# Performance work log

Measured on AMD Instinct MI355X. Metric: run time of the kernel, lower is better.

## Reference

```python
import jax, jax.numpy as jnp
import numpy as np


def setup_inputs() -> dict:
    key = jax.random.key(0)
    k1, k2, k3, k4 = jax.random.split(key, 4)
    B, T, D, U = 64, 2048, 256, 256
    X = jax.random.normal(k1, (B, T, D), dtype=jnp.float32)
    # scale weights ~ Glorot-ish so activations stay in range
    kernel = jax.random.normal(k2, (D, 3 * U), dtype=jnp.float32) / np.sqrt(D)
    recurrent_kernel = jax.random.normal(k3, (U, 3 * U), dtype=jnp.float32) / np.sqrt(U)
    bias = jax.random.normal(k4, (3 * U,), dtype=jnp.float32) * 0.01
    return {"X": X, "kernel": kernel, "recurrent_kernel": recurrent_kernel, "bias": bias}


def reference(X, kernel, recurrent_kernel, bias):
    # X: [B, T, D]; kernel: [D, 3U]; recurrent_kernel: [U, 3U]; bias: [3U]
    U = recurrent_kernel.shape[0]
    B = X.shape[0]
    Uz = recurrent_kernel[:, :U]
    Ur = recurrent_kernel[:, U:2 * U]
    Uh = recurrent_kernel[:, 2 * U:]
    # Precompute input projections for all timesteps in one GEMM (same math
    # as per-step matmul(x, W*) + B*).
    proj = X @ kernel + bias            # [B, T, 3U]
    proj = jnp.swapaxes(proj, 0, 1)     # [T, B, 3U] for scan over time
    xz = proj[:, :, :U]
    xr = proj[:, :, U:2 * U]
    xh = proj[:, :, 2 * U:]

    def step(a, xs):
        tz, tr, th = xs                  # each [B, U]
        z = jax.nn.sigmoid(a @ Uz + tz)
        r = jax.nn.sigmoid(a @ Ur + tr)
        h = jnp.tanh((r * a) @ Uh + th)
        a = z * a + (1.0 - z) * h
        return a, None

    a0 = jnp.zeros((B, U), dtype=X.dtype)
    a_final, _ = jax.lax.scan(step, a0, (xz, xr, xh))
    return a_final  # [B, U]
```

## Files before the change

### kernel.cpp

```cpp
#include <hip/hip_runtime.h>


typedef _Float16 half2_t __attribute__((ext_vector_type(2)));
typedef _Float16 half8_t __attribute__((ext_vector_type(8)));
typedef float    float4_t __attribute__((ext_vector_type(4)));

#define T_LEN 2048
#define B_SZ  64
#define D_IN  256
#define N3    768
#define U_SZ  256

#define H2(v, p) __builtin_shufflevector((v), (v), 2*(p), 2*(p)+1)

__device__ __forceinline__ float fdot2f(half2_t a, half2_t b, float c) {
#if __has_builtin(__builtin_amdgcn_fdot2)
    return __builtin_amdgcn_fdot2(a, b, c, false);
#else
    return c + (float)a[0]*(float)b[0] + (float)a[1]*(float)b[1];
#endif
}

__device__ __forceinline__ float fast_sigmoid(float s) {
    return __builtin_amdgcn_rcpf(1.0f + __builtin_amdgcn_exp2f(-1.44269504f * s));
}
__device__ __forceinline__ float fast_tanh(float s) {
    return 1.0f - 2.0f * __builtin_amdgcn_rcpf(1.0f + __builtin_amdgcn_exp2f(2.88539008f * s));
}

#define GA_LD 264
#define NT_N  16
#define MT_M  2048

__global__ __launch_bounds__(256) void proj_gemm(
    const float* __restrict__ X, const float* __restrict__ W,
    const float* __restrict__ bias, _Float16* __restrict__ proj)
{
    __shared__ __align__(16) _Float16 Ah[64 * GA_LD];
    __shared__ __align__(16) _Float16 Wh[48 * GA_LD];

    unsigned bid = blockIdx.x;
    unsigned idx = bid >> 3;
    unsigned mt  = (bid & 7) * (MT_M / 8) + (idx >> 4);
    unsigned nt  = idx & (NT_N - 1);
    int m0 = mt * 64, n0 = nt * 48;
    int tid = threadIdx.x;

    {
        int r = tid >> 6;
        int k = (tid & 63) * 4;
        #pragma unroll
        for (int i = 0; i < 16; ++i) {
            int row = i * 4 + r;
            float4_t v = *(const float4_t*)(X + (size_t)(m0 + row) * D_IN + k);
            _Float16* p = Ah + row * GA_LD + k;
            p[0] = (_Float16)v.x; p[1] = (_Float16)v.y;
            p[2] = (_Float16)v.z; p[3] = (_Float16)v.w;
        }
    }
    {
        int c  = tid & 63;
        int kk = tid >> 6;
        if (c < 48) {
            #pragma unroll 4
            for (int i = 0; i < 64; ++i) {
                int krow = i * 4 + kk;
                Wh[c * GA_LD + krow] = (_Float16)W[(size_t)krow * N3 + n0 + c];
            }
        }
    }
    __syncthreads();

    int r0 = (tid >> 4) << 2;
    int c  = tid & 15;
    float acc[4][3];
    #pragma unroll
    for (int rr = 0; rr < 4; ++rr)
        #pragma unroll
        for (int cc = 0; cc < 3; ++cc) acc[rr][cc] = 0.0f;

    for (int j = 0; j < 32; ++j) {
        half8_t av[4], wv[3];
        #pragma unroll
        for (int rr = 0; rr < 4; ++rr)
            av[rr] = *(const half8_t*)(Ah + (r0 + rr) * GA_LD + j * 8);
        #pragma unroll
        for (int cc = 0; cc < 3; ++cc)
            wv[cc] = *(const half8_t*)(Wh + (c + 16 * cc) * GA_LD + j * 8);
        #pragma unroll
        for (int rr = 0; rr < 4; ++rr)
            #pragma unroll
            for (int cc = 0; cc < 3; ++cc) {
                acc[rr][cc] = fdot2f(H2(av[rr],0), H2(wv[cc],0), acc[rr][cc]);
                acc[rr][cc] = fdot2f(H2(av[rr],1), H2(wv[cc],1), acc[rr][cc]);
                acc[rr][cc] = fdot2f(H2(av[rr],2), H2(wv[cc],2), acc[rr][cc]);
                acc[rr][cc] = fdot2f(H2(av[rr],3), H2(wv[cc],3), acc[rr][cc]);
            }
    }

    float bv[3];
    #pragma unroll
    for (int cc = 0; cc < 3; ++cc) bv[cc] = bias[n0 + c + 16 * cc];
    #pragma unroll
    for (int rr = 0; rr < 4; ++rr)
        #pragma unroll
        for (int cc = 0; cc < 3; ++cc)
            proj[(size_t)(m0 + r0 + rr) * N3 + (n0 + c + 16 * cc)] =
                (_Float16)(acc[rr][cc] + bv[cc]);
}

__global__ __launch_bounds__(768) void gru_scan(
    const float* __restrict__ RK, const _Float16* __restrict__ proj,
    float* __restrict__ out)
{
    __shared__ __align__(16) _Float16 aH[U_SZ];
    __shared__ __align__(16) _Float16 raH[U_SZ];
    __shared__ float zS[U_SZ];
    __shared__ float aF[U_SZ];

    const int b   = blockIdx.x;
    const int tid = threadIdx.x;
    const int g   = tid >> 8;
    const int u   = tid & 255;

    half2_t wcol[128];
    {
        const float* wp = RK + (size_t)(g << 8) + u;
        #pragma unroll
        for (int k2 = 0; k2 < 128; ++k2) {
            half2_t h;
            h[0] = (_Float16)wp[(size_t)(2 * k2)     * N3];
            h[1] = (_Float16)wp[(size_t)(2 * k2 + 1) * N3];
            wcol[k2] = h;
        }
    }

    if (tid < U_SZ) { aF[tid] = 0.0f; aH[tid] = (_Float16)0.0f; }

    const _Float16* px = proj + ((size_t)b * T_LEN) * N3 + (g << 8) + u;
    float xv = (float)px[0];
    __syncthreads();

    for (int t = 0; t < T_LEN; ++t) {
        const float x_cur = xv;
        if (t + 1 < T_LEN) xv = (float)px[(size_t)(t + 1) * N3];

        if (g < 2) {
            float acc = 0.0f;
            #pragma unroll
            for (int j = 0; j < 32; ++j) {
                half8_t av = *(const half8_t*)(aH + j * 8);
                acc = fdot2f(H2(av,0), wcol[4*j+0], acc);
                acc = fdot2f(H2(av,1), wcol[4*j+1], acc);
                acc = fdot2f(H2(av,2), wcol[4*j+2], acc);
                acc = fdot2f(H2(av,3), wcol[4*j+3], acc);
            }
            float sig = fast_sigmoid(acc + x_cur);
            if (g == 0) zS[u]  = sig;
            else        raH[u] = (_Float16)(sig * aF[u]);
        }
        __syncthreads();

        if (g == 2) {
            float acc = 0.0f;
            #pragma unroll
            for (int j = 0; j < 32; ++j) {
                half8_t rv = *(const half8_t*)(raH + j * 8);
                acc = fdot2f(H2(rv,0), wcol[4*j+0], acc);
                acc = fdot2f(H2(rv,1), wcol[4*j+1], acc);
                acc = fdot2f(H2(rv,2), wcol[4*j+2], acc);
                acc = fdot2f(H2(rv,3), wcol[4*j+3], acc);
            }
            float h  = fast_tanh(acc + x_cur);
            float z  = zS[u];
            float an = z * aF[u] + (1.0f - z) * h;
            aF[u] = an;
            aH[u] = (_Float16)an;
        }
        __syncthreads();
    }

    if (g == 0) out[(size_t)b * U_SZ + u] = aF[u];
}

extern "C" void kernel_launch(void* const* d_in, const int* in_sizes, int n_in,
                              void* d_out, int out_size, void* d_ws, size_t ws_size,
                              hipStream_t stream)
{
    const float* X    = (const float*)d_in[0];
    const float* W    = (const float*)d_in[1];
    const float* RK   = (const float*)d_in[2];
    const float* bias = (const float*)d_in[3];
    _Float16* proj = (_Float16*)d_ws;

    proj_gemm<<<MT_M * NT_N, 256, 0, stream>>>(X, W, bias, proj);
    gru_scan<<<B_SZ, 768, 0, stream>>>(RK, proj, (float*)d_out);
}
```

Before: 3.911 ms.

## Split candidate-gate matvec across all threads with K-halving and shuffle reduction

The GRU scan drops from 768 to 512 threads. In phase 2 every thread now computes half of the candidate-gate dot product (128 K-elements) and pairs combine their halves with a lane shuffle, so the third group no longer serializes the Uh matvec while two-thirds of threads idle. Accumulation also uses four independent partial sums to shorten fdot2 dependency chains. The cost is more registers per thread (192 half2 weight registers), which risks spills under the tighter launch bounds.

Measured after the change: 3.717 ms. 5.0% less time.

```diff
diff --git a/kernel.cpp b/kernel.cpp
--- a/kernel.cpp
+++ b/kernel.cpp
@@ -109,7 +109,7 @@
                 (_Float16)(acc[rr][cc] + bv[cc]);
 }
 
-__global__ __launch_bounds__(768) void gru_scan(
+__global__ __launch_bounds__(512, 2) void gru_scan(
     const float* __restrict__ RK, const _Float16* __restrict__ proj,
     float* __restrict__ out)
 {
@@ -118,12 +118,14 @@
     __shared__ float zS[U_SZ];
     __shared__ float aF[U_SZ];
 
-    const int b   = blockIdx.x;
-    const int tid = threadIdx.x;
-    const int g   = tid >> 8;
-    const int u   = tid & 255;
-
-    half2_t wcol[128];
+    const int b    = blockIdx.x;
+    const int tid  = threadIdx.x;
+    const int g    = tid >> 8;
+    const int u    = tid & 255;
+    const int hcol = tid >> 1;
+    const int kh   = tid & 1;
+
+    half2_t wA[128];
     {
         const float* wp = RK + (size_t)(g << 8) + u;
         #pragma unroll
@@ -131,56 +133,77 @@
             half2_t h;
             h[0] = (_Float16)wp[(size_t)(2 * k2)     * N3];
             h[1] = (_Float16)wp[(size_t)(2 * k2 + 1) * N3];
-            wcol[k2] = h;
+            wA[k2] = h;
+        }
+    }
+    half2_t wB[64];
+    {
+        const float* wq = RK + (size_t)(kh * 128) * N3 + 512 + hcol;
+        #pragma unroll
+        for (int k2 = 0; k2 < 64; ++k2) {
+            half2_t h;
+            h[0] = (_Float16)wq[(size_t)(2 * k2)     * N3];
+            h[1] = (_Float16)wq[(size_t)(2 * k2 + 1) * N3];
+            wB[k2] = h;
         }
     }
 
     if (tid < U_SZ) { aF[tid] = 0.0f; aH[tid] = (_Float16)0.0f; }
 
-    const _Float16* px = proj + ((size_t)b * T_LEN) * N3 + (g << 8) + u;
-    float xv = (float)px[0];
+    const _Float16* px1 = proj + ((size_t)b * T_LEN) * N3 + (g << 8) + u;
+    const _Float16* px2 = proj + ((size_t)b * T_LEN) * N3 + 512 + hcol;
+    float x1 = (float)px1[0];
+    float x2 = (float)px2[0];
     __syncthreads();
 
     for (int t = 0; t < T_LEN; ++t) {
-        const float x_cur = xv;
-        if (t + 1 < T_LEN) xv = (float)px[(size_t)(t + 1) * N3];
-
-        if (g < 2) {
-            float acc = 0.0f;
+        const float x1c = x1, x2c = x2;
+        if (t + 1 < T_LEN) {
+            x1 = (float)px1[(size_t)(t + 1) * N3];
+            x2 = (float)px2[(size_t)(t + 1) * N3];
+        }
+
+        {
+            float a0 = 0.f, a1 = 0.f, a2 = 0.f, a3 = 0.f;
             #pragma unroll
             for (int j = 0; j < 32; ++j) {
                 half8_t av = *(const half8_t*)(aH + j * 8);
-                acc = fdot2f(H2(av,0), wcol[4*j+0], acc);
-                acc = fdot2f(H2(av,1), wcol[4*j+1], acc);
-                acc = fdot2f(H2(av,2), wcol[4*j+2], acc);
-                acc = fdot2f(H2(av,3), wcol[4*j+3], acc);
-            }
-            float sig = fast_sigmoid(acc + x_cur);
+                a0 = fdot2f(H2(av,0), wA[4*j+0], a0);
+                a1 = fdot2f(H2(av,1), wA[4*j+1], a1);
+                a2 = fdot2f(H2(av,2), wA[4*j+2], a2);
+                a3 = fdot2f(H2(av,3), wA[4*j+3], a3);
+            }
+            float sig = fast_sigmoid((a0 + a1) + (a2 + a3) + x1c);
             if (g == 0) zS[u]  = sig;
             else        raH[u] = (_Float16)(sig * aF[u]);
         }
         __syncthreads();
 
-        if (g == 2) {
-            float acc = 0.0f;
+        {
+            float b0 = 0.f, b1 = 0.f, b2 = 0.f, b3 = 0.f;
+            const _Float16* rbase = raH + (kh << 7);
             #pragma unroll
-            for (int j = 0; j < 32; ++j) {
-                half8_t rv = *(const half8_t*)(raH + j * 8);
-                acc = fdot2f(H2(rv,0), wcol[4*j+0], acc);
-                acc = fdot2f(H2(rv,1), wcol[4*j+1], acc);
-                acc = fdot2f(H2(rv,2), wcol[4*j+2], acc);
-                acc = fdot2f(H2(rv,3), wcol[4*j+3], acc);
-            }
-            float h  = fast_tanh(acc + x_cur);
-            float z  = zS[u];
-            float an = z * aF[u] + (1.0f - z) * h;
-            aF[u] = an;
-            aH[u] = (_Float16)an;
+            for (int j = 0; j < 16; ++j) {
+                half8_t rv = *(const half8_t*)(rbase + j * 8);
+                b0 = fdot2f(H2(rv,0), wB[4*j+0], b0);
+                b1 = fdot2f(H2(rv,1), wB[4*j+1], b1);
+                b2 = fdot2f(H2(rv,2), wB[4*j+2], b2);
+                b3 = fdot2f(H2(rv,3), wB[4*j+3], b3);
+            }
+            float hs = (b0 + b1) + (b2 + b3);
+            hs += __shfl_xor(hs, 1, 64);
+            if (kh == 0) {
+                float h  = fast_tanh(hs + x2c);
+                float z  = zS[hcol];
+                float an = z * aF[hcol] + (1.0f - z) * h;
+                aF[hcol] = an;
+                aH[hcol] = (_Float16)an;
+            }
         }
         __syncthreads();
     }
 
-    if (g == 0) out[(size_t)b * U_SZ + u] = aF[u];
+    if (tid < U_SZ) out[(size_t)b * U_SZ + tid] = aF[tid];
 }
 
 extern "C" void kernel_launch(void* const* d_in, const int* in_sizes, int n_in,
@@ -194,5 +217,5 @@
     _Float16* proj = (_Float16*)d_ws;
 
     proj_gemm<<<MT_M * NT_N, 256, 0, stream>>>(X, W, bias, proj);
-    gru_scan<<<B_SZ, 768, 0, stream>>>(RK, proj, (float*)d_out);
-}
+    gru_scan<<<B_SZ, 512, 0, stream>>>(RK, proj, (float*)d_out);
+}
```
